# Performance work log

Measured on AMD Instinct MI355X. Metric: run time of the kernel, lower is better.

The kernel has to match this reference:

```python
import math
import jax, jax.numpy as jnp
import numpy as np

B, L, D, H = 4, 2048, 1024, 16
KD = D // H

def setup_inputs() -> dict:
    key = jax.random.key(0)
    k1, k2, k3 = jax.random.split(key, 3)
    x = jax.random.normal(k1, (B, L, D), dtype=jnp.float32)
    pad_mask = jnp.zeros((B, L), dtype=bool)  # True = padded (masked) key position
    w_qkv = jax.random.normal(k2, (D, 3 * D), dtype=jnp.float32) / math.sqrt(D)
    w_out = jax.random.normal(k3, (D, D), dtype=jnp.float32) / math.sqrt(D)
    return {"x": x, "pad_mask": pad_mask, "w_qkv": w_qkv, "w_out": w_out}

def reference(x, pad_mask, w_qkv, w_out):
    Bx, Lx, Dx = x.shape
    qkv = jnp.einsum('bld,de->ble', x, w_qkv)          # [B,L,3D]
    q, k, v = jnp.split(qkv, 3, axis=-1)
    def heads(t):
        return t.reshape(Bx, Lx, H, KD).transpose(0, 2, 1, 3)  # [B,H,L,kd]
    qh, kh, vh = heads(q), heads(k), heads(v)
    scores = jnp.einsum('bhqd,bhkd->bhqk', qh, kh) / math.sqrt(KD)
    causal = jnp.triu(jnp.ones((Lx, Lx), dtype=bool), k=1)[None, None]   # [1,1,L,L]
    mask = causal | pad_mask[:, None, None, :]                            # [B,1,L,L]
    scores = jnp.where(mask, -jnp.inf, scores)
    probs = jax.nn.softmax(scores, axis=-1)
    att = jnp.einsum('bhqk,bhkd->bhqd', probs, vh)
    concat = att.transpose(0, 2, 1, 3).reshape(Bx, Lx, Dx)
    return jnp.einsum('bld,de->ble', concat, w_out)
```

## Files before the change

### kernel.cpp

```cpp
#include <hip/hip_runtime.h>
#include <hip/hip_bf16.h>
#include <math.h>


typedef __bf16 bf16x8 __attribute__((ext_vector_type(8)));
typedef float f32x4 __attribute__((ext_vector_type(4)));

__device__ __forceinline__ f32x4 mfma16(bf16x8 a, bf16x8 b, f32x4 c) {
    return __builtin_amdgcn_mfma_f32_16x16x32_bf16(a, b, c, 0, 0, 0);
}

__device__ __forceinline__ void async16(const void* g, void* l) {
    __builtin_amdgcn_global_load_lds(
        (const __attribute__((address_space(1))) unsigned int*)g,
        (__attribute__((address_space(3))) unsigned int*)l, 16, 0, 0);
}

__global__ void cvt_f32_bf16_v4(const float* __restrict__ in,
                                __hip_bfloat16* __restrict__ out, int n4) {
    int i = blockIdx.x * blockDim.x + threadIdx.x;
    if (i >= n4) return;
    float4 v = ((const float4*)in)[i];
    __hip_bfloat16 t[4];
    t[0] = __float2bfloat16(v.x);
    t[1] = __float2bfloat16(v.y);
    t[2] = __float2bfloat16(v.z);
    t[3] = __float2bfloat16(v.w);
    ((uint2*)out)[i] = *(uint2*)t;
}

__global__ void transpose_cvt(const float* __restrict__ W,
                              __hip_bfloat16* __restrict__ Wt, int K, int N) {
    __shared__ float tile[32][33];
    int tid = threadIdx.x;
    int tx = tid & 31, ty = tid >> 5;
    int n0 = blockIdx.x * 32, k0 = blockIdx.y * 32;
#pragma unroll
    for (int i = 0; i < 4; ++i)
        tile[ty + 8 * i][tx] = W[(size_t)(k0 + ty + 8 * i) * N + n0 + tx];
    __syncthreads();
#pragma unroll
    for (int i = 0; i < 4; ++i)
        Wt[(size_t)(n0 + ty + 8 * i) * K + k0 + tx] =
            __float2bfloat16(tile[tx][ty + 8 * i]);
}

template <int MODE>
__global__ __launch_bounds__(256) void gemm_bf16(
    const __hip_bfloat16* __restrict__ A, const __hip_bfloat16* __restrict__ Bt,
    float* __restrict__ Cf, __hip_bfloat16* __restrict__ Qo,
    __hip_bfloat16* __restrict__ Ko, __hip_bfloat16* __restrict__ Vto, int M,
    int N, int K) {
    __shared__ __hip_bfloat16 As[128 * 64];
    __shared__ __hip_bfloat16 Bs[128 * 64];
    int tid = threadIdx.x;
    int wave = tid >> 6, lane = tid & 63;
    int quad = lane >> 4, l16 = lane & 15;
    int m0 = blockIdx.x * 128, n0 = blockIdx.y * 128;
    int wm = (wave >> 1) * 64, wn = (wave & 1) * 64;
    int srow = lane >> 3;
    int g8 = ((lane & 7) ^ srow) * 8;
    int swz = (l16 & 7);
    f32x4 acc[4][4] = {};
    for (int k0 = 0; k0 < K; k0 += 64) {
        __syncthreads();
#pragma unroll
        for (int j = 0; j < 4; ++j) {
            int r0 = (j * 4 + wave) * 8;
            async16(&A[(size_t)(m0 + r0 + srow) * K + k0 + g8], &As[r0 * 64]);
            async16(&Bt[(size_t)(n0 + r0 + srow) * K + k0 + g8], &Bs[r0 * 64]);
        }
        __syncthreads();
        bf16x8 af[2][4], bfr[2][4];
#pragma unroll
        for (int c = 0; c < 2; ++c) {
            int pg = ((c * 4 + quad) ^ swz) * 8;
#pragma unroll
            for (int i = 0; i < 4; ++i) {
                af[c][i]  = *(const bf16x8*)&As[(wm + i * 16 + l16) * 64 + pg];
                bfr[c][i] = *(const bf16x8*)&Bs[(wn + i * 16 + l16) * 64 + pg];
            }
        }
#pragma unroll
        for (int c = 0; c < 2; ++c)
#pragma unroll
            for (int mi = 0; mi < 4; ++mi)
#pragma unroll
                for (int ni = 0; ni < 4; ++ni)
                    acc[mi][ni] = mfma16(af[c][mi], bfr[c][ni], acc[mi][ni]);
    }
#pragma unroll
    for (int mi = 0; mi < 4; ++mi) {
#pragma unroll
        for (int ni = 0; ni < 4; ++ni) {
            int row0 = m0 + wm + mi * 16 + quad * 4;
            int col = n0 + wn + ni * 16 + l16;
            if (MODE == 0) {
#pragma unroll
                for (int r = 0; r < 4; ++r)
                    Cf[(size_t)(row0 + r) * N + col] = acc[mi][ni][r];
            } else {
                int which = col >> 10, hd = col & 1023;
                int h = hd >> 6, d = hd & 63;
                if (which == 0) {
#pragma unroll
                    for (int r = 0; r < 4; ++r) {
                        int row = row0 + r;
                        int b = row >> 11, l = row & 2047;
                        Qo[(((size_t)b * 16 + h) * 2048 + l) * 64 + d] =
                            __float2bfloat16(acc[mi][ni][r] * 0.18033688011f);
                    }
                } else if (which == 1) {
#pragma unroll
                    for (int r = 0; r < 4; ++r) {
                        int row = row0 + r;
                        int b = row >> 11, l = row & 2047;
                        Ko[(((size_t)b * 16 + h) * 2048 + l) * 64 + d] =
                            __float2bfloat16(acc[mi][ni][r]);
                    }
                } else {
                    int b = row0 >> 11, l = row0 & 2047;
                    __hip_bfloat16 t4[4];
#pragma unroll
                    for (int r = 0; r < 4; ++r)
                        t4[r] = __float2bfloat16(acc[mi][ni][r]);
                    *(uint2*)&Vto[(((size_t)b * 16 + h) * 64 + d) * 2048 + l] =
                        *(uint2*)t4;
                }
            }
        }
    }
}

__global__ __launch_bounds__(256) void attn_kernel(
    const __hip_bfloat16* __restrict__ Q, const __hip_bfloat16* __restrict__ Kk,
    const __hip_bfloat16* __restrict__ Vt,
    const unsigned char* __restrict__ pm, __hip_bfloat16* __restrict__ Ao) {
    __shared__ __hip_bfloat16 Ks[64 * 64];
    __shared__ __hip_bfloat16 Vs[64 * 64];
    constexpr int LDP = 72;
    __shared__ __hip_bfloat16 Ps[4 * 16 * LDP];
    __shared__ unsigned char pmS[2048];
    int tid = threadIdx.x;
    int wave = tid >> 6, lane = tid & 63;
    int quad = lane >> 4, l16 = lane & 15;
    int srow = lane >> 3;
    int g8 = ((lane & 7) ^ srow) * 8;
    int swz = (l16 & 7);
    int bx = blockIdx.x;
    int bh = blockIdx.y;
    int b = bh >> 4, h = bh & 15;
    const __hip_bfloat16* Qbh = Q + (size_t)bh * 2048 * 64;
    const __hip_bfloat16* Kbh = Kk + (size_t)bh * 2048 * 64;
    const __hip_bfloat16* Vbh = Vt + (size_t)bh * 64 * 2048;
    *(uint2*)&pmS[tid * 8] = *(const uint2*)&pm[b * 2048 + tid * 8];
    __hip_bfloat16* Pw = Ps + wave * 16 * LDP;

#pragma unroll
    for (int ph = 0; ph < 2; ++ph) {
        int qt = ph ? bx : 31 - bx;
        int q0 = qt * 64;
        bf16x8 qf[2];
        {
            int qrow = q0 + wave * 16 + l16;
            qf[0] = *(const bf16x8*)&Qbh[(size_t)qrow * 64 + quad * 8];
            qf[1] = *(const bf16x8*)&Qbh[(size_t)qrow * 64 + 32 + quad * 8];
        }
        f32x4 ov[4] = {};
        float lacc[4] = {};
        for (int kt = 0; kt <= qt; ++kt) {
            __syncthreads();
#pragma unroll
            for (int j = 0; j < 2; ++j) {
                int r0 = (j * 4 + wave) * 8;
                async16(&Kbh[((size_t)kt * 64 + r0 + srow) * 64 + g8],
                        &Ks[r0 * 64]);
                async16(&Vbh[(size_t)(r0 + srow) * 2048 + kt * 64 + g8],
                        &Vs[r0 * 64]);
            }
            __syncthreads();
            float sc[4][4];
#pragma unroll
            for (int kn = 0; kn < 4; ++kn) {
                int row = (kn * 16 + l16) * 64;
                bf16x8 b0 = *(const bf16x8*)&Ks[row + ((quad ^ swz) * 8)];
                bf16x8 b1 = *(const bf16x8*)&Ks[row + (((4 + quad) ^ swz) * 8)];
                float bias = pmS[kt * 64 + kn * 16 + l16] ? -INFINITY : -8.0f;
                f32x4 s = {};
                s = mfma16(qf[0], b0, s);
                s = mfma16(qf[1], b1, s);
#pragma unroll
                for (int r = 0; r < 4; ++r) sc[kn][r] = s[r] + bias;
            }
            if (kt == qt) {
                int qbase = wave * 16 + quad * 4;
#pragma unroll
                for (int kn = 0; kn < 4; ++kn) {
                    int key = kn * 16 + l16;
#pragma unroll
                    for (int r = 0; r < 4; ++r)
                        if (key > qbase + r) sc[kn][r] = -INFINITY;
                }
            }
#pragma unroll
            for (int kn = 0; kn < 4; ++kn)
#pragma unroll
                for (int r = 0; r < 4; ++r) {
                    float p = __builtin_amdgcn_exp2f(sc[kn][r]);
                    __hip_bfloat16 pb = __float2bfloat16(p);
                    Pw[(quad * 4 + r) * LDP + kn * 16 + l16] = pb;
                    lacc[r] += __bfloat162float(pb);
                }
            bf16x8 pf0 = *(const bf16x8*)&Pw[l16 * LDP + quad * 8];
            bf16x8 pf1 = *(const bf16x8*)&Pw[l16 * LDP + 32 + quad * 8];
#pragma unroll
            for (int ni = 0; ni < 4; ++ni) {
                int row = (ni * 16 + l16) * 64;
                bf16x8 v0 = *(const bf16x8*)&Vs[row + ((quad ^ swz) * 8)];
                bf16x8 v1 = *(const bf16x8*)&Vs[row + (((4 + quad) ^ swz) * 8)];
                ov[ni] = mfma16(pf0, v0, ov[ni]);
                ov[ni] = mfma16(pf1, v1, ov[ni]);
            }
        }
#pragma unroll
        for (int r = 0; r < 4; ++r) {
            float rs = lacc[r];
#pragma unroll
            for (int off = 1; off < 16; off <<= 1) rs += __shfl_xor(rs, off);
            float inv = 1.0f / rs;
            int qrow = q0 + wave * 16 + quad * 4 + r;
#pragma unroll
            for (int ni = 0; ni < 4; ++ni)
                Ao[(size_t)(b * 2048 + qrow) * 1024 + h * 64 + ni * 16 + l16] =
                    __float2bfloat16(ov[ni][r] * inv);
        }
    }
}

extern "C" void kernel_launch(void* const* d_in, const int* in_sizes, int n_in,
                              void* d_out, int out_size, void* d_ws,
                              size_t ws_size, hipStream_t stream) {
    (void)in_sizes; (void)n_in; (void)out_size; (void)ws_size;
    const float* x = (const float*)d_in[0];
    const unsigned char* pm = (const unsigned char*)d_in[1];
    const float* wqkv = (const float*)d_in[2];
    const float* wout = (const float*)d_in[3];
    float* out = (float*)d_out;

    char* p = (char*)d_ws;
    auto alloc = [&](size_t bytes) {
        char* q = p;
        p += (bytes + 255) & ~(size_t)255;
        return q;
    };
    __hip_bfloat16* xb    = (__hip_bfloat16*)alloc((size_t)8192 * 1024 * 2);
    __hip_bfloat16* wqkvT = (__hip_bfloat16*)alloc((size_t)3072 * 1024 * 2);
    __hip_bfloat16* woutT = (__hip_bfloat16*)alloc((size_t)1024 * 1024 * 2);
    __hip_bfloat16* qws   = (__hip_bfloat16*)alloc((size_t)8192 * 1024 * 2);
    __hip_bfloat16* kws   = (__hip_bfloat16*)alloc((size_t)8192 * 1024 * 2);
    __hip_bfloat16* vtws  = (__hip_bfloat16*)alloc((size_t)8192 * 1024 * 2);
    __hip_bfloat16* attb  = (__hip_bfloat16*)alloc((size_t)8192 * 1024 * 2);

    cvt_f32_bf16_v4<<<8192, 256, 0, stream>>>(x, xb, 8192 * 1024 / 4);
    transpose_cvt<<<dim3(3072 / 32, 1024 / 32), 256, 0, stream>>>(wqkv, wqkvT,
                                                                  1024, 3072);
    transpose_cvt<<<dim3(1024 / 32, 1024 / 32), 256, 0, stream>>>(wout, woutT,
                                                                  1024, 1024);
    gemm_bf16<1><<<dim3(64, 24), 256, 0, stream>>>(xb, wqkvT, nullptr, qws, kws,
                                                   vtws, 8192, 3072, 1024);
    attn_kernel<<<dim3(16, 64), 256, 0, stream>>>(qws, kws, vtws, pm, attb);
    gemm_bf16<0><<<dim3(64, 8), 256, 0, stream>>>(attb, woutT, out, nullptr,
                                                  nullptr, nullptr, 8192, 1024,
                                                  1024);
}
```

Measured before the change: 257.8 us.

## Use 128-row query tiles per block with reordered 1D grid in attention

```diff
diff --git a/kernel.cpp b/kernel.cpp
--- a/kernel.cpp
+++ b/kernel.cpp
@@ -132,14 +132,14 @@
     }
 }
 
-__global__ __launch_bounds__(256) void attn_kernel(
+__global__ __launch_bounds__(256, 4) void attn_kernel(
     const __hip_bfloat16* __restrict__ Q, const __hip_bfloat16* __restrict__ Kk,
     const __hip_bfloat16* __restrict__ Vt,
     const unsigned char* __restrict__ pm, __hip_bfloat16* __restrict__ Ao) {
     __shared__ __hip_bfloat16 Ks[64 * 64];
     __shared__ __hip_bfloat16 Vs[64 * 64];
     constexpr int LDP = 72;
-    __shared__ __hip_bfloat16 Ps[4 * 16 * LDP];
+    __shared__ __hip_bfloat16 Ps[4 * 32 * LDP];
     __shared__ unsigned char pmS[2048];
     int tid = threadIdx.x;
     int wave = tid >> 6, lane = tid & 63;
@@ -147,94 +147,109 @@
     int srow = lane >> 3;
     int g8 = ((lane & 7) ^ srow) * 8;
     int swz = (l16 & 7);
-    int bx = blockIdx.x;
-    int bh = blockIdx.y;
+    int lin = blockIdx.x;
+    int bh = (lin & 7) * 8 + ((lin >> 3) & 7);
+    int qt = 15 - (lin >> 6);
     int b = bh >> 4, h = bh & 15;
     const __hip_bfloat16* Qbh = Q + (size_t)bh * 2048 * 64;
     const __hip_bfloat16* Kbh = Kk + (size_t)bh * 2048 * 64;
     const __hip_bfloat16* Vbh = Vt + (size_t)bh * 64 * 2048;
     *(uint2*)&pmS[tid * 8] = *(const uint2*)&pm[b * 2048 + tid * 8];
-    __hip_bfloat16* Pw = Ps + wave * 16 * LDP;
-
-#pragma unroll
-    for (int ph = 0; ph < 2; ++ph) {
-        int qt = ph ? bx : 31 - bx;
-        int q0 = qt * 64;
-        bf16x8 qf[2];
-        {
-            int qrow = q0 + wave * 16 + l16;
-            qf[0] = *(const bf16x8*)&Qbh[(size_t)qrow * 64 + quad * 8];
-            qf[1] = *(const bf16x8*)&Qbh[(size_t)qrow * 64 + 32 + quad * 8];
-        }
-        f32x4 ov[4] = {};
-        float lacc[4] = {};
-        for (int kt = 0; kt <= qt; ++kt) {
-            __syncthreads();
-#pragma unroll
-            for (int j = 0; j < 2; ++j) {
-                int r0 = (j * 4 + wave) * 8;
-                async16(&Kbh[((size_t)kt * 64 + r0 + srow) * 64 + g8],
-                        &Ks[r0 * 64]);
-                async16(&Vbh[(size_t)(r0 + srow) * 2048 + kt * 64 + g8],
-                        &Vs[r0 * 64]);
-            }
-            __syncthreads();
-            float sc[4][4];
-#pragma unroll
-            for (int kn = 0; kn < 4; ++kn) {
-                int row = (kn * 16 + l16) * 64;
-                bf16x8 b0 = *(const bf16x8*)&Ks[row + ((quad ^ swz) * 8)];
-                bf16x8 b1 = *(const bf16x8*)&Ks[row + (((4 + quad) ^ swz) * 8)];
-                float bias = pmS[kt * 64 + kn * 16 + l16] ? -INFINITY : -8.0f;
-                f32x4 s = {};
-                s = mfma16(qf[0], b0, s);
-                s = mfma16(qf[1], b1, s);
-#pragma unroll
-                for (int r = 0; r < 4; ++r) sc[kn][r] = s[r] + bias;
-            }
-            if (kt == qt) {
-                int qbase = wave * 16 + quad * 4;
-#pragma unroll
-                for (int kn = 0; kn < 4; ++kn) {
-                    int key = kn * 16 + l16;
-#pragma unroll
-                    for (int r = 0; r < 4; ++r)
-                        if (key > qbase + r) sc[kn][r] = -INFINITY;
+    __hip_bfloat16* Pw = Ps + wave * 32 * LDP;
+    int q0 = qt * 128;
+    bf16x8 qf[2][2];
+#pragma unroll
+    for (int mi = 0; mi < 2; ++mi) {
+        int qrow = q0 + (wave + 4 * mi) * 16 + l16;
+        qf[mi][0] = *(const bf16x8*)&Qbh[(size_t)qrow * 64 + quad * 8];
+        qf[mi][1] = *(const bf16x8*)&Qbh[(size_t)qrow * 64 + 32 + quad * 8];
+    }
+    f32x4 ov[2][4] = {};
+    float lacc[2][4] = {};
+    int ktmax = 2 * qt + 1;
+    for (int kt = 0; kt <= ktmax; ++kt) {
+        __syncthreads();
+#pragma unroll
+        for (int j = 0; j < 2; ++j) {
+            int r0 = (j * 4 + wave) * 8;
+            async16(&Kbh[((size_t)kt * 64 + r0 + srow) * 64 + g8], &Ks[r0 * 64]);
+            async16(&Vbh[(size_t)(r0 + srow) * 2048 + kt * 64 + g8],
+                    &Vs[r0 * 64]);
+        }
+        __syncthreads();
+#pragma unroll
+        for (int hk = 0; hk < 2; ++hk) {
+            float sc[2][2][4];
+#pragma unroll
+            for (int kn = 0; kn < 2; ++kn) {
+                int krow = ((hk * 2 + kn) * 16 + l16) * 64;
+                bf16x8 b0 = *(const bf16x8*)&Ks[krow + ((quad ^ swz) * 8)];
+                bf16x8 b1 = *(const bf16x8*)&Ks[krow + (((4 + quad) ^ swz) * 8)];
+                float bias =
+                    pmS[kt * 64 + (hk * 2 + kn) * 16 + l16] ? -INFINITY : -8.0f;
+#pragma unroll
+                for (int mi = 0; mi < 2; ++mi) {
+                    f32x4 s = {};
+                    s = mfma16(qf[mi][0], b0, s);
+                    s = mfma16(qf[mi][1], b1, s);
+#pragma unroll
+                    for (int r = 0; r < 4; ++r) sc[mi][kn][r] = s[r] + bias;
                 }
             }
-#pragma unroll
-            for (int kn = 0; kn < 4; ++kn)
-#pragma unroll
-                for (int r = 0; r < 4; ++r) {
-                    float p = __builtin_amdgcn_exp2f(sc[kn][r]);
-                    __hip_bfloat16 pb = __float2bfloat16(p);
-                    Pw[(quad * 4 + r) * LDP + kn * 16 + l16] = pb;
-                    lacc[r] += __bfloat162float(pb);
+            if (kt == 2 * qt || kt == ktmax) {
+#pragma unroll
+                for (int mi = 0; mi < 2; ++mi) {
+                    int qbase = q0 + (wave + 4 * mi) * 16 + quad * 4;
+#pragma unroll
+                    for (int kn = 0; kn < 2; ++kn) {
+                        int key = kt * 64 + (hk * 2 + kn) * 16 + l16;
+#pragma unroll
+                        for (int r = 0; r < 4; ++r)
+                            if (key > qbase + r) sc[mi][kn][r] = -INFINITY;
+                    }
                 }
-            bf16x8 pf0 = *(const bf16x8*)&Pw[l16 * LDP + quad * 8];
-            bf16x8 pf1 = *(const bf16x8*)&Pw[l16 * LDP + 32 + quad * 8];
+            }
+#pragma unroll
+            for (int mi = 0; mi < 2; ++mi)
+#pragma unroll
+                for (int kn = 0; kn < 2; ++kn)
+#pragma unroll
+                    for (int r = 0; r < 4; ++r) {
+                        float p = __builtin_amdgcn_exp2f(sc[mi][kn][r]);
+                        Pw[(mi * 16 + quad * 4 + r) * LDP + (hk * 2 + kn) * 16 +
+                           l16] = __float2bfloat16(p);
+                        lacc[mi][r] += p;
+                    }
+            bf16x8 pf[2];
+#pragma unroll
+            for (int mi = 0; mi < 2; ++mi)
+                pf[mi] = *(const bf16x8*)&Pw[(mi * 16 + l16) * LDP + hk * 32 +
+                                             quad * 8];
 #pragma unroll
             for (int ni = 0; ni < 4; ++ni) {
-                int row = (ni * 16 + l16) * 64;
-                bf16x8 v0 = *(const bf16x8*)&Vs[row + ((quad ^ swz) * 8)];
-                bf16x8 v1 = *(const bf16x8*)&Vs[row + (((4 + quad) ^ swz) * 8)];
-                ov[ni] = mfma16(pf0, v0, ov[ni]);
-                ov[ni] = mfma16(pf1, v1, ov[ni]);
-            }
-        }
+                int vrow = (ni * 16 + l16) * 64;
+                bf16x8 v =
+                    *(const bf16x8*)&Vs[vrow + (((hk * 4 + quad) ^ swz) * 8)];
+#pragma unroll
+                for (int mi = 0; mi < 2; ++mi)
+                    ov[mi][ni] = mfma16(pf[mi], v, ov[mi][ni]);
+            }
+        }
+    }
+#pragma unroll
+    for (int mi = 0; mi < 2; ++mi)
 #pragma unroll
         for (int r = 0; r < 4; ++r) {
-            float rs = lacc[r];
+            float rs = lacc[mi][r];
 #pragma unroll
             for (int off = 1; off < 16; off <<= 1) rs += __shfl_xor(rs, off);
             float inv = 1.0f / rs;
-            int qrow = q0 + wave * 16 + quad * 4 + r;
+            int qrow = q0 + (wave + 4 * mi) * 16 + quad * 4 + r;
 #pragma unroll
             for (int ni = 0; ni < 4; ++ni)
                 Ao[(size_t)(b * 2048 + qrow) * 1024 + h * 64 + ni * 16 + l16] =
-                    __float2bfloat16(ov[ni][r] * inv);
-        }
-    }
+                    __float2bfloat16(ov[mi][ni][r] * inv);
+        }
 }
 
 extern "C" void kernel_launch(void* const* d_in, const int* in_sizes, int n_in,
@@ -268,7 +283,7 @@
                                                                   1024, 1024);
     gemm_bf16<1><<<dim3(64, 24), 256, 0, stream>>>(xb, wqkvT, nullptr, qws, kws,
                                                    vtws, 8192, 3072, 1024);
-    attn_kernel<<<dim3(16, 64), 256, 0, stream>>>(qws, kws, vtws, pm, attb);
+    attn_kernel<<<1024, 256, 0, stream>>>(qws, kws, vtws, pm, attb);
     gemm_bf16<0><<<dim3(64, 8), 256, 0, stream>>>(attb, woutT, out, nullptr,
                                                   nullptr, nullptr, 8192, 1024,
                                                   1024);
```

Result: faster. 242.3 us (-6.0%).
